# Performance work log

Measured on AMD Instinct MI355X. Metric: run time of the kernel, lower is better.

Reference implementation:

```python
import jax, jax.numpy as jnp
import numpy as np

NUM_HEADS = 8


def setup_inputs() -> dict:
    key = jax.random.key(0)
    ks = jax.random.split(key, 8)
    B, N, D, H = 4, 1200, 256, NUM_HEADS
    return {
        "query_bbox": jax.random.normal(ks[0], (B, N, 10), jnp.float32) * 20.0,
        "query_feat": jax.random.normal(ks[1], (B, N, D), jnp.float32),
        "beta_w": jax.random.normal(ks[2], (H, D), jnp.float32) * 0.02,
        "beta_b": jax.random.uniform(ks[3], (H,), jnp.float32, 0.0, 2.0),
        "in_proj_w": jax.random.normal(ks[4], (3 * D, D), jnp.float32) * (D ** -0.5),
        "in_proj_b": jnp.zeros((3 * D,), jnp.float32),
        "out_proj_w": jax.random.normal(ks[5], (D, D), jnp.float32) * (D ** -0.5),
        "out_proj_b": jnp.zeros((D,), jnp.float32),
    }


def reference(query_bbox, query_feat, beta_w, beta_b, in_proj_w, in_proj_b,
              out_proj_w, out_proj_b):
    B, N, D = query_feat.shape
    H = NUM_HEADS
    hd = D // H

    # center_dists (no_grad in original): negative pairwise L2 of bbox centers
    centers = jax.lax.stop_gradient(query_bbox[..., :2])            # [B,N,2]
    diff = centers[:, :, None, :] - centers[:, None, :, :]          # [B,N,N,2]
    dist = -jnp.sqrt(jnp.sum(diff * diff, axis=-1))                 # [B,N,N]

    # per-head learned beta scale
    beta = jnp.einsum('bnd,hd->bhn', query_feat, beta_w) + beta_b[None, :, None]  # [B,H,N]
    attn_mask = dist[:, None, :, :] * beta[..., None]               # [B,H,N,N]

    # multi-head self-attention with additive mask
    qkv = jnp.einsum('bnd,ed->bne', query_feat, in_proj_w) + in_proj_b
    q, k, v = jnp.split(qkv, 3, axis=-1)
    q = q.reshape(B, N, H, hd)
    k = k.reshape(B, N, H, hd)
    v = v.reshape(B, N, H, hd)

    scores = jnp.einsum('bqhd,bkhd->bhqk', q, k) * (hd ** -0.5) + attn_mask
    attn = jax.nn.softmax(scores, axis=-1)                          # [B,H,N,N]
    out = jnp.einsum('bhqk,bkhd->bqhd', attn, v).reshape(B, N, D)
    return jnp.einsum('bnd,ed->bne', out, out_proj_w) + out_proj_b
```

## Files before the change

### kernel.cpp

```cpp
#include <hip/hip_runtime.h>
#include <hip/hip_bf16.h>

#define BC 4
#define NQ 1200
#define DIM 256
#define NH 8
#define HD 32
#define E3 768
#define MROWS (BC*NQ)
#define SCALE 0.17677669529663687f
#define L2E 1.4426950408889634f
#define SL2E (SCALE * L2E)

#define VT2_PER_BH 40960
#define VT2_PER_HH 20480

typedef __attribute__((ext_vector_type(8))) short bf16x8;
typedef __attribute__((ext_vector_type(4))) float f32x4;
typedef __attribute__((ext_vector_type(2))) unsigned u32x2;

__device__ inline short f2bf(float f) {
    __hip_bfloat16 h = __float2bfloat16(f);
    return *reinterpret_cast<short*>(&h);
}
__device__ inline unsigned pack2bf(float a, float b) {
    unsigned ua = (unsigned short)f2bf(a);
    unsigned ub = (unsigned short)f2bf(b);
    return ua | (ub << 16);
}

__global__ void beta_ctr_kernel(const float* __restrict__ feat, const float* __restrict__ bw,
                                const float* __restrict__ bb, const float* __restrict__ bbox,
                                float* __restrict__ beta, float* __restrict__ ctr) {
    int gw = (blockIdx.x * 256 + threadIdx.x) >> 6;
    int lane = threadIdx.x & 63;
    if (gw >= MROWS) return;
    const float* frow = feat + (size_t)gw * DIM;
    float acc[NH];
#pragma unroll
    for (int h = 0; h < NH; ++h) acc[h] = 0.f;
#pragma unroll
    for (int it = 0; it < DIM / 64; ++it) {
        int d = it * 64 + lane;
        float f = frow[d];
#pragma unroll
        for (int h = 0; h < NH; ++h) acc[h] += f * bw[h * DIM + d];
    }
#pragma unroll
    for (int h = 0; h < NH; ++h) {
#pragma unroll
        for (int off = 32; off; off >>= 1) acc[h] += __shfl_xor(acc[h], off);
    }
    int b = gw / NQ, n = gw % NQ;
#pragma unroll
    for (int h = 0; h < NH; ++h) {
        float v = acc[h] + bb[h];
        if (lane == h) beta[(b * NH + h) * NQ + n] = v;
    }
    if (lane == 0) {
        ctr[gw * 2]     = bbox[(size_t)gw * 10];
        ctr[gw * 2 + 1] = bbox[(size_t)gw * 10 + 1];
    }
}

template<bool AF32, bool BF32, bool OUTF32, bool VTOUT, bool QSCALE>
__global__ __launch_bounds__(256) void gemm_k256(const void* __restrict__ Av,
                                                 const void* __restrict__ Bv,
                                                 const float* __restrict__ bias,
                                                 void* __restrict__ Cout, int Edim,
                                                 short* __restrict__ vtout) {
    __shared__ short as[64][40];
    __shared__ short bs[64][40];
    int m0 = blockIdx.y * 64, e0 = blockIdx.x * 64;
    int t = threadIdx.x, lane = t & 63, wid = t >> 6;
    int wr = (wid >> 1) * 32, wc = (wid & 1) * 32;
    f32x4 acc[2][2] = {};
    int lrow = t >> 2, lch = t & 3;
    const float qs = (QSCALE && e0 < DIM) ? SL2E : 1.f;

    for (int ks = 0; ks < DIM / 32; ++ks) {
        bf16x8 av, wv;
        if (AF32) {
            const float* A = (const float*)Av;
            float4 f0 = *(const float4*)(A + (size_t)(m0 + lrow) * DIM + ks * 32 + lch * 8);
            float4 f1 = *(const float4*)(A + (size_t)(m0 + lrow) * DIM + ks * 32 + lch * 8 + 4);
            av[0]=f2bf(f0.x); av[1]=f2bf(f0.y); av[2]=f2bf(f0.z); av[3]=f2bf(f0.w);
            av[4]=f2bf(f1.x); av[5]=f2bf(f1.y); av[6]=f2bf(f1.z); av[7]=f2bf(f1.w);
        } else {
            av = *(const bf16x8*)((const short*)Av + (size_t)(m0 + lrow) * DIM + ks * 32 + lch * 8);
        }
        if (BF32) {
            const float* B = (const float*)Bv;
            float4 f0 = *(const float4*)(B + (size_t)(e0 + lrow) * DIM + ks * 32 + lch * 8);
            float4 f1 = *(const float4*)(B + (size_t)(e0 + lrow) * DIM + ks * 32 + lch * 8 + 4);
            wv[0]=f2bf(f0.x*qs); wv[1]=f2bf(f0.y*qs); wv[2]=f2bf(f0.z*qs); wv[3]=f2bf(f0.w*qs);
            wv[4]=f2bf(f1.x*qs); wv[5]=f2bf(f1.y*qs); wv[6]=f2bf(f1.z*qs); wv[7]=f2bf(f1.w*qs);
        } else {
            wv = *(const bf16x8*)((const short*)Bv + (size_t)(e0 + lrow) * DIM + ks * 32 + lch * 8);
        }
        __syncthreads();
        *(bf16x8*)&as[lrow][lch * 8] = av;
        *(bf16x8*)&bs[lrow][lch * 8] = wv;
        __syncthreads();
#pragma unroll
        for (int sm = 0; sm < 2; ++sm) {
            bf16x8 af = *(const bf16x8*)&as[wr + sm * 16 + (lane & 15)][(lane >> 4) * 8];
#pragma unroll
            for (int sn = 0; sn < 2; ++sn) {
                bf16x8 bfv = *(const bf16x8*)&bs[wc + sn * 16 + (lane & 15)][(lane >> 4) * 8];
                acc[sm][sn] = __builtin_amdgcn_mfma_f32_16x16x32_bf16(af, bfv, acc[sm][sn], 0, 0, 0);
            }
        }
    }
#pragma unroll
    for (int sm = 0; sm < 2; ++sm)
#pragma unroll
        for (int sn = 0; sn < 2; ++sn) {
            int e = e0 + wc + sn * 16 + (lane & 15);
            float bv = bias[e];
            if (QSCALE && e < DIM) bv *= SL2E;
            float vals[4];
            int mbase = m0 + wr + sm * 16 + (lane >> 4) * 4;
#pragma unroll
            for (int r = 0; r < 4; ++r) vals[r] = acc[sm][sn][r] + bv;
            if (VTOUT && e >= 2 * DIM) {
                int dv = e - 2 * DIM;
                int hv = dv >> 5, dd = dv & 31;
                int hh = dd >> 4, di = dd & 15;
                int bb = mbase / NQ, nn = mbase - bb * NQ;
                short4 o;
                o.x = f2bf(vals[0]); o.y = f2bf(vals[1]);
                o.z = f2bf(vals[2]); o.w = f2bf(vals[3]);
                size_t off = (size_t)(bb * NH + hv) * VT2_PER_BH + hh * VT2_PER_HH
                           + (nn >> 3) * 128 + di * 8 + (nn & 7);
                *(short4*)&vtout[off] = o;
            } else {
#pragma unroll
                for (int r = 0; r < 4; ++r) {
                    int m = mbase + r;
                    if (OUTF32) ((float*)Cout)[(size_t)m * Edim + e] = vals[r];
                    else        ((short*)Cout)[(size_t)m * Edim + e] = f2bf(vals[r]);
                }
            }
        }
}

#define BUFSZ 17408
#define KT_OFF 0
#define VT_OFF 8192
#define CK_OFF 16384
#define PL_OFF (2*BUFSZ)
__global__ __launch_bounds__(256, 4) void attn_kernel(const short* __restrict__ qkv,
                                                      const short* __restrict__ vt2,
                                                      const float* __restrict__ beta,
                                                      const float* __restrict__ ctr,
                                                      short* __restrict__ attnb) {
    __shared__ __align__(16) char smem[2 * BUFSZ + 4096];

    const int t = threadIdx.x, lane = t & 63, w = t >> 6;
    const int g = lane >> 4, i = lane & 15;
    const int qg = w >> 1, ksp = w & 1;
    const int bh = blockIdx.y, b = bh >> 3, h = bh & 7;
    const int q0 = blockIdx.x * 32 + qg * 16;
    const int q = q0 + i, qc = min(q, NQ - 1);
    const int kwb = ksp * 64;
    const int bq = b * NQ;

    bf16x8 qf = *(const bf16x8*)(qkv + (size_t)(bq + qc) * E3 + h * HD + g * 8);
    const float cqx = ctr[(bq + qc) * 2];
    const float cqy = ctr[(bq + qc) * 2 + 1];
    const float nbql = -beta[(b * NH + h) * NQ + qc] * L2E;

    float mcur = 0.f, lsum = 0.f;
    f32x4 o0 = {}, o1 = {};

    const int koff = ((t >> 6) << 4) + (t & 15);
    const short* kld0 = qkv + (size_t)bq * E3 + DIM + h * HD + (size_t)koff * E3 + ((t >> 4) & 3) * 8;
    const short* kld1 = kld0 + (size_t)64 * E3;
    const short* vld0 = vt2 + (size_t)bh * VT2_PER_BH + (((t >> 4) & 15)) * 128 + (t & 15) * 8;
    const short* vld1 = vld0 + VT2_PER_HH;
    const float* cld = ctr + (size_t)bq * 2 + t * 2;

    bf16x8 sk0, sk1, sv0, sv1;
    float2 sc2;
    auto stage_load = [&]() {
        sk0 = *(const bf16x8*)kld0;
        sk1 = *(const bf16x8*)kld1;
        sv0 = *(const bf16x8*)vld0;
        sv1 = *(const bf16x8*)vld1;
        if (t < 128) sc2 = *(const float2*)cld;
        kld0 += (size_t)128 * E3; kld1 += (size_t)128 * E3;
        vld0 += 2048; vld1 += 2048; cld += 256;
    };
    auto stage_write = [&](int base) {
        *(bf16x8*)&smem[base + KT_OFF + t * 16]         = sk0;
        *(bf16x8*)&smem[base + KT_OFF + (t + 256) * 16] = sk1;
        *(bf16x8*)&smem[base + VT_OFF + t * 16]         = sv0;
        *(bf16x8*)&smem[base + VT_OFF + (t + 256) * 16] = sv1;
        if (t < 128) *(float2*)&smem[base + CK_OFF + t * 8] = sc2;
    };

    stage_load();
    stage_write(0);
    __syncthreads();
    int cur = 0;

    for (int kb = 0; kb < NQ; kb += 128) {
        const bool haveNext = (kb + 128 < NQ);
        const bool tail = (kb + 128 > NQ);
        if (haveNext) stage_load();

        const int cb = cur * BUFSZ;
        float st[16];
        f32x4 cinit = {-mcur, -mcur, -mcur, -mcur};
#pragma unroll
        for (int kcl = 0; kcl < 4; ++kcl) {
            bf16x8 af = *(const bf16x8*)&smem[cb + KT_OFF + (((ksp * 4 + kcl) * 64 + lane) << 4)];
            f32x4 s = __builtin_amdgcn_mfma_f32_16x16x32_bf16(af, qf, cinit, 0, 0, 0);
            int lk = kwb + kcl * 16 + 4 * g;
            float4 cA = *(const float4*)&smem[cb + CK_OFF + lk * 8];
            float4 cB = *(const float4*)&smem[cb + CK_OFF + lk * 8 + 16];
            float cxv[4] = {cA.x, cA.z, cB.x, cB.z};
            float cyv[4] = {cA.y, cA.w, cB.y, cB.w};
#pragma unroll
            for (int r = 0; r < 4; ++r) {
                float dx = cqx - cxv[r], dy = cqy - cyv[r];
                float d2 = __builtin_fmaf(dx, dx, dy * dy);
                float dist = __builtin_amdgcn_sqrtf(d2);
                st[kcl * 4 + r] = __builtin_fmaf(dist, nbql, s[r]);
            }
            if (tail) {
#pragma unroll
                for (int r = 0; r < 4; ++r)
                    if (kb + lk + r >= NQ) st[kcl * 4 + r] = -1e30f;
            }
        }

        float a0 = fmaxf(fmaxf(st[0],  st[1]),  st[2]);
        float a1 = fmaxf(fmaxf(st[3],  st[4]),  st[5]);
        float a2 = fmaxf(fmaxf(st[6],  st[7]),  st[8]);
        float a3 = fmaxf(fmaxf(st[9],  st[10]), st[11]);
        float a4 = fmaxf(fmaxf(st[12], st[13]), st[14]);
        float vm = fmaxf(fmaxf(fmaxf(a0, a1), a2), fmaxf(fmaxf(a3, a4), st[15]));
        vm = fmaxf(vm, __shfl_xor(vm, 16));
        vm = fmaxf(vm, __shfl_xor(vm, 32));
        if (!__all(vm <= 8.0f)) {
            float dm = fmaxf(vm, 0.f);
            float al = __builtin_amdgcn_exp2f(-dm);
            mcur += dm;
            lsum *= al;
#pragma unroll
            for (int r = 0; r < 4; ++r) { o0[r] *= al; o1[r] *= al; }
#pragma unroll
            for (int x = 0; x < 16; ++x) st[x] -= dm;
        }
#pragma unroll
        for (int x = 0; x < 16; ++x) st[x] = __builtin_amdgcn_exp2f(st[x]);
        float s0 = (st[0] + st[1]) + (st[2] + st[3]);
        float s1 = (st[4] + st[5]) + (st[6] + st[7]);
        float s2 = (st[8] + st[9]) + (st[10] + st[11]);
        float s3 = (st[12] + st[13]) + (st[14] + st[15]);
        float rs = (s0 + s1) + (s2 + s3);
        rs += __shfl_xor(rs, 16);
        rs += __shfl_xor(rs, 32);
        lsum += rs;

#pragma unroll
        for (int kc2 = 0; kc2 < 2; ++kc2) {
#pragma unroll
            for (int kk = 0; kk < 2; ++kk) {
                int kcl = 2 * kc2 + kk;
                u32x2 pw = {pack2bf(st[kcl * 4 + 0], st[kcl * 4 + 1]),
                            pack2bf(st[kcl * 4 + 2], st[kcl * 4 + 3])};
                *(u32x2*)&smem[PL_OFF + (w << 10) + (((kk << 1) + (g >> 1)) << 8) + (i << 4) + ((g & 1) << 3)] = pw;
            }
            bf16x8 pbf = *(const bf16x8*)&smem[PL_OFF + (w << 10) + (g << 8) + (i << 4)];
            int vidx = (8 * ksp + 4 * kc2 + g) * 16 + i;
            bf16x8 vf0 = *(const bf16x8*)&smem[cb + VT_OFF + (vidx << 4)];
            bf16x8 vf1 = *(const bf16x8*)&smem[cb + VT_OFF + ((256 + vidx) << 4)];
            o0 = __builtin_amdgcn_mfma_f32_16x16x32_bf16(vf0, pbf, o0, 0, 0, 0);
            o1 = __builtin_amdgcn_mfma_f32_16x16x32_bf16(vf1, pbf, o1, 0, 0, 0);
        }

        if (haveNext) stage_write((cur ^ 1) * BUFSZ);
        __syncthreads();
        cur ^= 1;
    }

    float* mrg = (float*)smem;
    float* my = mrg + (w * 64 + lane) * 10;
    my[0] = mcur; my[1] = lsum;
#pragma unroll
    for (int r = 0; r < 4; ++r) { my[2 + r] = o0[r]; my[6 + r] = o1[r]; }
    __syncthreads();
    const float* pr = mrg + ((w ^ 1) * 64 + lane) * 10;
    float m2 = pr[0], l2 = pr[1];
    float mN = fmaxf(mcur, m2);
    float a1 = __builtin_amdgcn_exp2f(mcur - mN);
    float a2 = __builtin_amdgcn_exp2f(m2 - mN);
    float inv = 1.f / (lsum * a1 + l2 * a2);
    int hh = w & 1;
    f32x4 mine = hh ? o1 : o0;
    if (q < NQ) {
        short4 outv;
        float vals[4];
#pragma unroll
        for (int r = 0; r < 4; ++r) vals[r] = (mine[r] * a1 + pr[2 + hh * 4 + r] * a2) * inv;
        outv.x = f2bf(vals[0]); outv.y = f2bf(vals[1]);
        outv.z = f2bf(vals[2]); outv.w = f2bf(vals[3]);
        *(short4*)&attnb[(size_t)(bq + q) * DIM + h * HD + hh * 16 + 4 * g] = outv;
    }
}

extern "C" void kernel_launch(void* const* d_in, const int* in_sizes, int n_in,
                              void* d_out, int out_size, void* d_ws, size_t ws_size,
                              hipStream_t stream) {
    const float* bbox  = (const float*)d_in[0];
    const float* feat  = (const float*)d_in[1];
    const float* bw    = (const float*)d_in[2];
    const float* bb    = (const float*)d_in[3];
    const float* in_w  = (const float*)d_in[4];
    const float* in_b  = (const float*)d_in[5];
    const float* out_w = (const float*)d_in[6];
    const float* out_b = (const float*)d_in[7];
    float* out = (float*)d_out;

    char* ws = (char*)d_ws;
    size_t off = 0;
    auto alloc = [&](size_t bytes) { void* p = ws + off; off += (bytes + 255) & ~255ull; return p; };
    short* qkvb  = (short*)alloc((size_t)MROWS * E3 * 2);
    short* vtb   = (short*)alloc((size_t)BC * NH * VT2_PER_BH * 2);
    short* attnb = (short*)alloc((size_t)MROWS * DIM * 2);
    float* betab = (float*)alloc((size_t)BC * NH * NQ * 4);
    float* ctr   = (float*)alloc((size_t)BC * NQ * 2 * 4 + 1024);
    (void)ws_size; (void)in_sizes; (void)n_in; (void)out_size;

    beta_ctr_kernel<<<MROWS / 4, 256, 0, stream>>>(feat, bw, bb, bbox, betab, ctr);
    gemm_k256<true, true, false, true, true><<<dim3(E3 / 64, MROWS / 64), 256, 0, stream>>>(feat, in_w, in_b, qkvb, E3, vtb);
    attn_kernel<<<dim3((NQ + 31) / 32, BC * NH), 256, 0, stream>>>(qkvb, vtb, betab, ctr, attnb);
    gemm_k256<false, true, true, false, false><<<dim3(DIM / 64, MROWS / 64), 256, 0, stream>>>(attnb, out_w, out_b, out, DIM, nullptr);
}
```

Measured before the change: 60.73 us.

## Stream K/V/center tiles directly into LDS and defer row-sum reductions

Replaces the register-staged global loads plus later LDS writes with global_load_lds direct-to-LDS transfers into the alternate buffer, removing register pressure and the explicit store pass. The row-max cross-lane shuffles now run only when a rescale is needed, and the row-sum shuffles move out of the loop to a single reduction at the end. Risks: the direct LDS writes need correct vmcnt waits before the barrier, and the center load now assumes 64 lanes times 16 bytes cover the tile.

```diff
diff --git a/kernel.cpp b/kernel.cpp
--- a/kernel.cpp
+++ b/kernel.cpp
@@ -27,6 +27,12 @@
     unsigned ua = (unsigned short)f2bf(a);
     unsigned ub = (unsigned short)f2bf(b);
     return ua | (ub << 16);
+}
+
+__device__ __forceinline__ void gll16(const void* g, void* l) {
+    __builtin_amdgcn_global_load_lds(
+        (const __attribute__((address_space(1))) unsigned*)g,
+        (__attribute__((address_space(3))) unsigned*)l, 16, 0, 0);
 }
 
 __global__ void beta_ctr_kernel(const float* __restrict__ feat, const float* __restrict__ bw,
@@ -179,36 +185,26 @@
     const short* kld1 = kld0 + (size_t)64 * E3;
     const short* vld0 = vt2 + (size_t)bh * VT2_PER_BH + (((t >> 4) & 15)) * 128 + (t & 15) * 8;
     const short* vld1 = vld0 + VT2_PER_HH;
-    const float* cld = ctr + (size_t)bq * 2 + t * 2;
-
-    bf16x8 sk0, sk1, sv0, sv1;
-    float2 sc2;
-    auto stage_load = [&]() {
-        sk0 = *(const bf16x8*)kld0;
-        sk1 = *(const bf16x8*)kld1;
-        sv0 = *(const bf16x8*)vld0;
-        sv1 = *(const bf16x8*)vld1;
-        if (t < 128) sc2 = *(const float2*)cld;
+    const char*  cld  = (const char*)(ctr + (size_t)bq * 2) + lane * 16;
+
+    auto stage_issue = [&](int base) {
+        gll16(kld0, &smem[base + KT_OFF + t * 16]);
+        gll16(kld1, &smem[base + KT_OFF + (t + 256) * 16]);
+        gll16(vld0, &smem[base + VT_OFF + t * 16]);
+        gll16(vld1, &smem[base + VT_OFF + (t + 256) * 16]);
+        if (w == 0) gll16(cld, &smem[base + CK_OFF + lane * 16]);
         kld0 += (size_t)128 * E3; kld1 += (size_t)128 * E3;
-        vld0 += 2048; vld1 += 2048; cld += 256;
+        vld0 += 2048; vld1 += 2048; cld += 1024;
     };
-    auto stage_write = [&](int base) {
-        *(bf16x8*)&smem[base + KT_OFF + t * 16]         = sk0;
-        *(bf16x8*)&smem[base + KT_OFF + (t + 256) * 16] = sk1;
-        *(bf16x8*)&smem[base + VT_OFF + t * 16]         = sv0;
-        *(bf16x8*)&smem[base + VT_OFF + (t + 256) * 16] = sv1;
-        if (t < 128) *(float2*)&smem[base + CK_OFF + t * 8] = sc2;
-    };
-
-    stage_load();
-    stage_write(0);
+
+    stage_issue(0);
     __syncthreads();
     int cur = 0;
 
     for (int kb = 0; kb < NQ; kb += 128) {
         const bool haveNext = (kb + 128 < NQ);
         const bool tail = (kb + 128 > NQ);
-        if (haveNext) stage_load();
+        if (haveNext) stage_issue((cur ^ 1) * BUFSZ);
 
         const int cb = cur * BUFSZ;
         float st[16];
@@ -242,10 +238,10 @@
         float a3 = fmaxf(fmaxf(st[9],  st[10]), st[11]);
         float a4 = fmaxf(fmaxf(st[12], st[13]), st[14]);
         float vm = fmaxf(fmaxf(fmaxf(a0, a1), a2), fmaxf(fmaxf(a3, a4), st[15]));
-        vm = fmaxf(vm, __shfl_xor(vm, 16));
-        vm = fmaxf(vm, __shfl_xor(vm, 32));
         if (!__all(vm <= 8.0f)) {
-            float dm = fmaxf(vm, 0.f);
+            float vr = fmaxf(vm, __shfl_xor(vm, 16));
+            vr = fmaxf(vr, __shfl_xor(vr, 32));
+            float dm = fmaxf(vr, 0.f);
             float al = __builtin_amdgcn_exp2f(-dm);
             mcur += dm;
             lsum *= al;
@@ -260,10 +256,7 @@
         float s1 = (st[4] + st[5]) + (st[6] + st[7]);
         float s2 = (st[8] + st[9]) + (st[10] + st[11]);
         float s3 = (st[12] + st[13]) + (st[14] + st[15]);
-        float rs = (s0 + s1) + (s2 + s3);
-        rs += __shfl_xor(rs, 16);
-        rs += __shfl_xor(rs, 32);
-        lsum += rs;
+        lsum += (s0 + s1) + (s2 + s3);
 
 #pragma unroll
         for (int kc2 = 0; kc2 < 2; ++kc2) {
@@ -282,11 +275,12 @@
             o1 = __builtin_amdgcn_mfma_f32_16x16x32_bf16(vf1, pbf, o1, 0, 0, 0);
         }
 
-        if (haveNext) stage_write((cur ^ 1) * BUFSZ);
         __syncthreads();
         cur ^= 1;
     }
 
+    lsum += __shfl_xor(lsum, 16);
+    lsum += __shfl_xor(lsum, 32);
     float* mrg = (float*)smem;
     float* my = mrg + (w * 64 + lane) * 10;
     my[0] = mcur; my[1] = lsum;
```

Result: no change. 61.86 us (+1.9%).
